# Kernel optimization log

Measured on AMD Instinct MI355X. Metric: run time of the kernel, lower is better.

Reference implementation:

```python
import jax, jax.numpy as jnp
import numpy as np

B, S, H = 4, 2048, 1024
E, K = 8, 2

def setup_inputs() -> dict:
    key = jax.random.key(0)
    ks = jax.random.split(key, 5)
    scale = 1.0 / np.sqrt(H)
    return {
        "x": jax.random.normal(ks[0], (B, S, H), dtype=jnp.float32),
        "router_w": jax.random.uniform(ks[1], (E, H), jnp.float32, -scale, scale),
        "router_b": jax.random.uniform(ks[2], (E,), jnp.float32, -scale, scale),
        "expert_w": jax.random.uniform(ks[3], (E, H, H), jnp.float32, -scale, scale),
        "expert_b": jax.random.uniform(ks[4], (E, H), jnp.float32, -scale, scale),
    }


def reference(x, router_w, router_b, expert_w, expert_b):
    # Router: [b,s,E]
    scores = jnp.einsum("bsh,eh->bse", x, router_w) + router_b
    probs = jax.nn.softmax(scores, axis=-1)
    p, expert_id = jax.lax.top_k(probs, K)          # [b,s,K]
    # Renormalize top-k probs (matches p / p.sum(dim=2))
    p = p / jnp.sum(p, axis=-1, keepdims=True)
    # Per-token combine weight per expert: [b,s,E]
    onehot = jax.nn.one_hot(expert_id, E, dtype=x.dtype)  # [b,s,K,E]
    w_comb = jnp.einsum("bske,bsk->bse", onehot, p)
    # All-expert linear (Linear: x @ W.T + b): [b,s,E,h]
    all_out = jnp.einsum("bsh,edh->bsed", x, expert_w) + expert_b
    # Weighted combine over selected experts: [b,s,h]
    return jnp.einsum("bse,bsed->bsd", w_comb, all_out)
```

## Files before the change

### kernel.cpp

```cpp
#include <hip/hip_runtime.h>
#include <hip/hip_bf16.h>
#include <math.h>

#define TOK 8192
#define HD 1024
#define NE 8
#define SLOTS 17408
#define NGRP 512
#define GRPSZ 16

typedef _Float16 half8 __attribute__((ext_vector_type(8)));
typedef _Float16 half4v __attribute__((ext_vector_type(4)));
typedef float floatx4 __attribute__((ext_vector_type(4)));

__global__ __launch_bounds__(256) void score_cvt(
    const float* __restrict__ x,
    const float* __restrict__ rw,
    const float* __restrict__ rb,
    const float* __restrict__ ew,
    _Float16* __restrict__ xh,
    _Float16* __restrict__ wh,
    int* __restrict__ epair,
    float* __restrict__ w1out,
    int* __restrict__ hist) {
  const int tid = threadIdx.x;
  const int blk = blockIdx.x;
  if (blk >= NGRP) {
    const int g = (blk - NGRP) * 256 + tid;
    const float4* src = (const float4*)ew;
    half4v* dst = (half4v*)wh;
#pragma unroll
    for (int j = 0; j < 4; ++j) {
      float4 v = src[g + 524288 * j];
      half4v h = {(_Float16)v.x, (_Float16)v.y, (_Float16)v.z, (_Float16)v.w};
      dst[g + 524288 * j] = h;
    }
    return;
  }
  const int lane = tid & 63;
  const int wid = tid >> 6;
  __shared__ int hcnt[NE];
  if (tid < NE) hcnt[tid] = 0;
  __syncthreads();

#pragma unroll
  for (int i = 0; i < 4; ++i) {
    const int t = blk * GRPSZ + wid * 4 + i;
    const float4* xp = (const float4*)(x + (size_t)t * HD);
    float4 xr[4];
#pragma unroll
    for (int k = 0; k < 4; ++k) xr[k] = xp[lane + 64 * k];
    _Float16* xo = xh + (size_t)t * HD;
#pragma unroll
    for (int k = 0; k < 4; ++k) {
      half4v h = {(_Float16)xr[k].x, (_Float16)xr[k].y,
                  (_Float16)xr[k].z, (_Float16)xr[k].w};
      *(half4v*)(xo + (lane + 64 * k) * 4) = h;
    }
    float sc[NE];
#pragma unroll
    for (int e = 0; e < NE; ++e) {
      const float4* wp = (const float4*)(rw + e * HD);
      float a = 0.f;
#pragma unroll
      for (int k = 0; k < 4; ++k) {
        float4 w = wp[lane + 64 * k];
        a += xr[k].x * w.x + xr[k].y * w.y + xr[k].z * w.z + xr[k].w * w.w;
      }
#pragma unroll
      for (int off = 32; off > 0; off >>= 1) a += __shfl_xor(a, off);
      sc[e] = a + rb[e];
    }
    float b1 = sc[0]; int e1 = 0;
#pragma unroll
    for (int e = 1; e < NE; ++e) if (sc[e] > b1) { b1 = sc[e]; e1 = e; }
    float b2 = -1e30f; int e2 = 0;
#pragma unroll
    for (int e = 0; e < NE; ++e) { if (e != e1 && sc[e] > b2) { b2 = sc[e]; e2 = e; } }
    if (lane == 0) {
      epair[t] = e1 | (e2 << 8);
      w1out[t] = 1.f / (1.f + expf(b2 - b1));
      atomicAdd(&hcnt[e1], 1);
      atomicAdd(&hcnt[e2], 1);
    }
  }
  __syncthreads();
  if (tid < NE) hist[tid * NGRP + blk] = hcnt[tid];
}

__global__ __launch_bounds__(256) void moe_scatter(
    const int* __restrict__ hist,
    const int* __restrict__ epair,
    const float* __restrict__ w1in,
    int* __restrict__ cntp,
    int* __restrict__ basep,
    int* __restrict__ tok_list,
    float* __restrict__ tok_w,
    int* __restrict__ slot_of) {
  const int tid = threadIdx.x;
  const int blk = blockIdx.x;
  __shared__ int pre_s[NE], tot_s[NE], alloc_s[NE];
  {
    const int e = tid >> 5;
    const int sl = tid & 31;
    int p = 0, tt = 0;
#pragma unroll
    for (int j = 0; j < 16; ++j) {
      int g = sl + 32 * j;
      int h = hist[e * NGRP + g];
      tt += h;
      p += (g < blk) ? h : 0;
    }
#pragma unroll
    for (int off = 16; off > 0; off >>= 1) {
      p += __shfl_xor(p, off);
      tt += __shfl_xor(tt, off);
    }
    if (sl == 0) { pre_s[e] = p; tot_s[e] = tt; }
  }
  __syncthreads();
  if (tid == 0) {
    int b = 0;
    for (int e = 0; e < NE; ++e) {
      alloc_s[e] = b + pre_s[e];
      if (blk == 0) { cntp[e * 64] = tot_s[e]; basep[e] = b; }
      b += (tot_s[e] + 127) & ~127;
    }
  }
  __syncthreads();
  if (tid < GRPSZ) {
    const int t = blk * GRPSZ + tid;
    int ep = epair[t];
    int e1 = ep & 0xff, e2 = ep >> 8;
    float w1 = w1in[t];
    int s1 = atomicAdd(&alloc_s[e1], 1);
    tok_list[s1] = t; tok_w[s1] = w1; slot_of[2 * t] = s1;
    int s2 = atomicAdd(&alloc_s[e2], 1);
    tok_list[s2] = t; tok_w[s2] = 1.f - w1; slot_of[2 * t + 1] = s2;
  }
}

template <int EPI>
__global__ __launch_bounds__(256, 2) void moe_gemm(
    const _Float16* __restrict__ Ah, const _Float16* __restrict__ Bh,
    const float* __restrict__ eb,
    const int* __restrict__ cntp, const int* __restrict__ base,
    const int* __restrict__ tok_list, const float* __restrict__ tok_w,
    _Float16* __restrict__ scratch, float* __restrict__ out) {
  const int e = blockIdx.z;
  const int ce = cntp[e * 64];
  const int mt = ((blockIdx.y >> 3) << 3) | blockIdx.x;
  const int m0 = mt << 7;
  if (m0 >= ce) return;
  const int n0 = (blockIdx.y & 7) << 7;
  const int sbase = base[e];
  const int tid = threadIdx.x;
  const int lane = tid & 63;
  const int wid = tid >> 6;
  const int wm = wid & 1, wn = wid >> 1;

  __shared__ _Float16 A_s[2][128 * 64];
  __shared__ _Float16 B_s[2][128 * 64];
  __shared__ int tok_s[128];
  __shared__ float w_s[128];

  if (tid < 128) {
    int tk = 0; float w = 0.f;
    if (m0 + tid < ce) { tk = tok_list[sbase + m0 + tid]; w = tok_w[sbase + m0 + tid]; }
    tok_s[tid] = tk; w_s[tid] = w;
  }
  __syncthreads();

  floatx4 acc[4][4];
  floatx4 zero = {0.f, 0.f, 0.f, 0.f};
#pragma unroll
  for (int i = 0; i < 4; ++i)
#pragma unroll
    for (int j = 0; j < 4; ++j) acc[i][j] = zero;

  const int wbase = e * HD * HD;
  const int rloc = lane >> 3, sub = lane & 7;
  int agoff[4], bgoff[4];
#pragma unroll
  for (int q = 0; q < 4; ++q) {
    int row = wid * 32 + q * 8 + rloc;
    int g = sub ^ (row & 7);
    agoff[q] = tok_s[row] * HD + g * 8;
    bgoff[q] = wbase + (n0 + row) * HD + g * 8;
  }
  const int l15 = lane & 15, q4 = lane >> 4;

  auto stage = [&](int buf, int k0) {
#pragma unroll
    for (int q = 0; q < 4; ++q) {
      const int r0 = wid * 32 + q * 8;
      __builtin_amdgcn_global_load_lds(
          (const __attribute__((address_space(1))) unsigned int*)(Ah + agoff[q] + k0),
          (__attribute__((address_space(3))) unsigned int*)&A_s[buf][r0 * 64], 16, 0, 0);
      __builtin_amdgcn_global_load_lds(
          (const __attribute__((address_space(1))) unsigned int*)(Bh + bgoff[q] + k0),
          (__attribute__((address_space(3))) unsigned int*)&B_s[buf][r0 * 64], 16, 0, 0);
    }
  };

  auto compute = [&](int buf) {
#pragma unroll
    for (int kf = 0; kf < 2; ++kf) {
      half8 afr[4], bfr[4];
      const int cc = kf * 4 + q4;
#pragma unroll
      for (int i = 0; i < 4; ++i)
        afr[i] = *(const half8*)&A_s[buf][(wm * 64 + i * 16 + l15) * 64 + ((cc ^ (l15 & 7)) * 8)];
#pragma unroll
      for (int j = 0; j < 4; ++j)
        bfr[j] = *(const half8*)&B_s[buf][(wn * 64 + j * 16 + l15) * 64 + ((cc ^ (l15 & 7)) * 8)];
#pragma unroll
      for (int i = 0; i < 4; ++i)
#pragma unroll
        for (int j = 0; j < 4; ++j)
          acc[i][j] = __builtin_amdgcn_mfma_f32_16x16x32_f16(afr[i], bfr[j], acc[i][j], 0, 0, 0);
    }
  };

  stage(0, 0);
  __syncthreads();
  for (int ks = 0; ks < 16; ks += 2) {
    stage(1, (ks + 1) * 64);
    compute(0);
    __syncthreads();
    if (ks < 14) stage(0, (ks + 2) * 64);
    compute(1);
    __syncthreads();
  }

#pragma unroll
  for (int j = 0; j < 4; ++j) {
    int col = n0 + wn * 64 + j * 16 + l15;
    float bias = eb[e * HD + col];
#pragma unroll
    for (int i = 0; i < 4; ++i) {
      int rbase = wm * 64 + i * 16 + (q4 << 2);
#pragma unroll
      for (int r = 0; r < 4; ++r) {
        int row = rbase + r;
        float v = w_s[row] * (acc[i][j][r] + bias);
        if (EPI == 1) {
          scratch[(size_t)(sbase + m0 + row) * HD + col] = (_Float16)v;
        } else {
          if (m0 + row < ce)
            atomicAdd(&out[(size_t)tok_s[row] * HD + col], v);
        }
      }
    }
  }
}

__global__ void moe_combine(const _Float16* __restrict__ scratch,
                            const int* __restrict__ slot_of,
                            float* __restrict__ out) {
  const int tid = threadIdx.x;
  const int t = blockIdx.x * 2 + (tid >> 7);
  const int c = (tid & 127) * 8;
  int sa = slot_of[2 * t], sb = slot_of[2 * t + 1];
  half8 a = *(const half8*)&scratch[(size_t)sa * HD + c];
  half8 b = *(const half8*)&scratch[(size_t)sb * HD + c];
  float* o = out + (size_t)t * HD + c;
  float4 o0 = {(float)a[0] + (float)b[0], (float)a[1] + (float)b[1],
               (float)a[2] + (float)b[2], (float)a[3] + (float)b[3]};
  float4 o1 = {(float)a[4] + (float)b[4], (float)a[5] + (float)b[5],
               (float)a[6] + (float)b[6], (float)a[7] + (float)b[7]};
  *(float4*)o = o0;
  *(float4*)(o + 4) = o1;
}

extern "C" void kernel_launch(void* const* d_in, const int* in_sizes, int n_in,
                              void* d_out, int out_size, void* d_ws, size_t ws_size,
                              hipStream_t stream) {
  (void)in_sizes; (void)n_in;
  const float* x  = (const float*)d_in[0];
  const float* rw = (const float*)d_in[1];
  const float* rb = (const float*)d_in[2];
  const float* ew = (const float*)d_in[3];
  const float* eb = (const float*)d_in[4];
  float* out = (float*)d_out;

  char* w = (char*)d_ws;
  int*   cntp     = (int*)(w + 0);
  int*   basep    = (int*)(w + 2048);
  int*   hist     = (int*)(w + 2304);
  size_t off = 2304 + (size_t)NE * NGRP * 4;
  int*   tok_list = (int*)(w + off);  off += (size_t)SLOTS * 4;
  float* tok_w    = (float*)(w + off); off += (size_t)SLOTS * 4;
  int*   slot_of  = (int*)(w + off);  off += (size_t)TOK * 8;
  int*   epair    = (int*)(w + off);  off += (size_t)TOK * 4;
  float* w1buf    = (float*)(w + off); off += (size_t)TOK * 4;
  off = (off + 255) & ~255ull;
  size_t xh_off = off;
  size_t wh_off = xh_off + (size_t)TOK * HD * 2;
  size_t scr_off = wh_off + (size_t)NE * HD * HD * 2;
  size_t needscr = scr_off + (size_t)SLOTS * HD * 2;
  bool fastscr = ws_size >= needscr;

  if (!fastscr)
    hipMemsetAsync(d_out, 0, (size_t)out_size * sizeof(float), stream);

  _Float16* xh = (_Float16*)(w + xh_off);
  _Float16* wh = (_Float16*)(w + wh_off);
  _Float16* scr = fastscr ? (_Float16*)(w + scr_off) : nullptr;

  score_cvt<<<NGRP + 2048, 256, 0, stream>>>(x, rw, rb, ew, xh, wh,
                                             epair, w1buf, hist);
  moe_scatter<<<NGRP, 256, 0, stream>>>(hist, epair, w1buf, cntp, basep,
                                        tok_list, tok_w, slot_of);

  dim3 grid(HD / 128, TOK / 128, NE);
  if (fastscr) {
    moe_gemm<1><<<grid, 256, 0, stream>>>(xh, wh, eb, cntp, basep,
                                          tok_list, tok_w, scr, out);
    moe_combine<<<TOK / 2, 256, 0, stream>>>(scr, slot_of, out);
  } else {
    moe_gemm<0><<<grid, 256, 0, stream>>>(xh, wh, eb, cntp, basep,
                                          tok_list, tok_w, nullptr, out);
  }
}
```

Baseline: 194.5 us.

## Single-buffer GEMM LDS for higher occupancy and reorder grid by expert

The MoE GEMM drops its double-buffered LDS staging in favour of one buffer, with a load, sync, compute, sync loop. This halves shared memory per block so launch bounds can target 4 blocks per CU instead of 2. The grid is also reshaped so the expert index is the fastest-varying block dimension, which changes the block dispatch order. The trade is losing explicit load/compute overlap within a block, relying on more resident waves to hide memory latency. The tighter register budget risks spills with the 64-register accumulator tile.

```diff
diff --git a/kernel.cpp b/kernel.cpp
--- a/kernel.cpp
+++ b/kernel.cpp
@@ -141,15 +141,15 @@
 }
 
 template <int EPI>
-__global__ __launch_bounds__(256, 2) void moe_gemm(
+__global__ __launch_bounds__(256, 4) void moe_gemm(
     const _Float16* __restrict__ Ah, const _Float16* __restrict__ Bh,
     const float* __restrict__ eb,
     const int* __restrict__ cntp, const int* __restrict__ base,
     const int* __restrict__ tok_list, const float* __restrict__ tok_w,
     _Float16* __restrict__ scratch, float* __restrict__ out) {
-  const int e = blockIdx.z;
+  const int e = blockIdx.x;
   const int ce = cntp[e * 64];
-  const int mt = ((blockIdx.y >> 3) << 3) | blockIdx.x;
+  const int mt = blockIdx.y >> 3;
   const int m0 = mt << 7;
   if (m0 >= ce) return;
   const int n0 = (blockIdx.y & 7) << 7;
@@ -159,8 +159,8 @@
   const int wid = tid >> 6;
   const int wm = wid & 1, wn = wid >> 1;
 
-  __shared__ _Float16 A_s[2][128 * 64];
-  __shared__ _Float16 B_s[2][128 * 64];
+  __shared__ _Float16 A_s[128 * 64];
+  __shared__ _Float16 B_s[128 * 64];
   __shared__ int tok_s[128];
   __shared__ float w_s[128];
 
@@ -190,30 +190,30 @@
   }
   const int l15 = lane & 15, q4 = lane >> 4;
 
-  auto stage = [&](int buf, int k0) {
+  auto stage = [&](int k0) {
 #pragma unroll
     for (int q = 0; q < 4; ++q) {
       const int r0 = wid * 32 + q * 8;
       __builtin_amdgcn_global_load_lds(
           (const __attribute__((address_space(1))) unsigned int*)(Ah + agoff[q] + k0),
-          (__attribute__((address_space(3))) unsigned int*)&A_s[buf][r0 * 64], 16, 0, 0);
+          (__attribute__((address_space(3))) unsigned int*)&A_s[r0 * 64], 16, 0, 0);
       __builtin_amdgcn_global_load_lds(
           (const __attribute__((address_space(1))) unsigned int*)(Bh + bgoff[q] + k0),
-          (__attribute__((address_space(3))) unsigned int*)&B_s[buf][r0 * 64], 16, 0, 0);
+          (__attribute__((address_space(3))) unsigned int*)&B_s[r0 * 64], 16, 0, 0);
     }
   };
 
-  auto compute = [&](int buf) {
+  auto compute = [&]() {
 #pragma unroll
     for (int kf = 0; kf < 2; ++kf) {
       half8 afr[4], bfr[4];
       const int cc = kf * 4 + q4;
 #pragma unroll
       for (int i = 0; i < 4; ++i)
-        afr[i] = *(const half8*)&A_s[buf][(wm * 64 + i * 16 + l15) * 64 + ((cc ^ (l15 & 7)) * 8)];
+        afr[i] = *(const half8*)&A_s[(wm * 64 + i * 16 + l15) * 64 + ((cc ^ (l15 & 7)) * 8)];
 #pragma unroll
       for (int j = 0; j < 4; ++j)
-        bfr[j] = *(const half8*)&B_s[buf][(wn * 64 + j * 16 + l15) * 64 + ((cc ^ (l15 & 7)) * 8)];
+        bfr[j] = *(const half8*)&B_s[(wn * 64 + j * 16 + l15) * 64 + ((cc ^ (l15 & 7)) * 8)];
 #pragma unroll
       for (int i = 0; i < 4; ++i)
 #pragma unroll
@@ -222,14 +222,10 @@
     }
   };
 
-  stage(0, 0);
-  __syncthreads();
-  for (int ks = 0; ks < 16; ks += 2) {
-    stage(1, (ks + 1) * 64);
-    compute(0);
+  for (int t = 0; t < 16; ++t) {
+    stage(t * 64);
     __syncthreads();
-    if (ks < 14) stage(0, (ks + 2) * 64);
-    compute(1);
+    compute();
     __syncthreads();
   }
 
@@ -313,7 +309,7 @@
   moe_scatter<<<NGRP, 256, 0, stream>>>(hist, epair, w1buf, cntp, basep,
                                         tok_list, tok_w, slot_of);
 
-  dim3 grid(HD / 128, TOK / 128, NE);
+  dim3 grid(NE, 512, 1);
   if (fastscr) {
     moe_gemm<1><<<grid, 256, 0, stream>>>(xh, wh, eb, cntp, basep,
                                           tok_list, tok_w, scr, out);
```

Result: faster. 183.4 us, median of 2 (-5.7%).
